# Performance work log

Hardware: AMD Instinct MI355X
Metric: run time of the kernel (lower is better)

The kernel has to match this reference:

```python
import jax, jax.numpy as jnp
import numpy as np

DIM = 192
HEADS = 6
WS = 8
SHIFT = 4
POS_DIM = 12  # (dim//4)//4
HIDDEN = 768
EPS = 1e-5


def _win_partition(x, ws):
    B, H, W, C = x.shape
    x = x.reshape(B, H // ws, ws, W // ws, ws, C)
    return x.transpose(0, 1, 3, 2, 4, 5).reshape(-1, ws, ws, C)


def _win_reverse(w, ws, H, W):
    B = w.shape[0] // ((H // ws) * (W // ws))
    x = w.reshape(B, H // ws, W // ws, ws, ws, -1)
    return x.transpose(0, 1, 3, 2, 4, 5).reshape(B, H, W, -1)


def _calc_mask(H, W, ws, shift):
    img = np.zeros((1, H, W, 1), np.float32)
    sl = (slice(0, -ws), slice(-ws, -shift), slice(-shift, None))
    cnt = 0
    for hs in sl:
        for wsl in sl:
            img[:, hs, wsl, :] = cnt
            cnt += 1
    mw = img.reshape(1, H // ws, ws, W // ws, ws, 1).transpose(0, 1, 3, 2, 4, 5).reshape(-1, ws * ws)
    am = mw[:, None, :] - mw[:, :, None]
    am = np.where(am != 0, -100.0, 0.0).astype(np.float32)
    return am  # [nW, N, N]


def _rel_index(ws):
    coords = np.stack(np.meshgrid(np.arange(ws), np.arange(ws), indexing='ij')).reshape(2, -1)
    rel = (coords[:, :, None] - coords[:, None, :]).transpose(1, 2, 0)
    rel[..., 0] += ws - 1
    rel[..., 1] += ws - 1
    rel[..., 0] *= 2 * ws - 1
    return rel.sum(-1)  # [N, N]


def _biases(ws):
    bh = np.arange(1 - ws, ws)
    bw = np.arange(1 - ws, ws)
    b = np.stack(np.meshgrid(bh, bw, indexing='ij')).reshape(2, -1).T
    return b.astype(np.float32)  # [(2ws-1)^2, 2]


def _ln(x, g, b):
    mu = jnp.mean(x, -1, keepdims=True)
    var = jnp.var(x, -1, keepdims=True)
    return (x - mu) / jnp.sqrt(var + EPS) * g + b


def setup_inputs() -> dict:
    key = jax.random.key(0)
    ks = jax.random.split(key, 20)
    B, L, C = 8, 128 * 128, DIM
    d = {
        'x': jax.random.normal(ks[0], (B, L, C), jnp.float32),
        'k_v': jnp.zeros((1,), jnp.float32),
        'H': 128, 'W': 128,
        'n1_g': jnp.ones((C,)), 'n1_b': jnp.zeros((C,)),
        'qkv_w': jax.random.normal(ks[1], (C, 3 * C)) * 0.02,
        'qkv_b': jnp.zeros((3 * C,)),
        'proj_w': jax.random.normal(ks[2], (C, C)) * 0.02,
        'proj_b': jnp.zeros((C,)),
        'pp_w': jax.random.normal(ks[3], (2, POS_DIM)) * 0.02,
        'pp_b': jnp.zeros((POS_DIM,)),
        'p1_g': jnp.ones((POS_DIM,)), 'p1_b': jnp.zeros((POS_DIM,)),
        'p1_w': jax.random.normal(ks[4], (POS_DIM, POS_DIM)) * 0.02,
        'p1_bias': jnp.zeros((POS_DIM,)),
        'p2_g': jnp.ones((POS_DIM,)), 'p2_b': jnp.zeros((POS_DIM,)),
        'p2_w': jax.random.normal(ks[5], (POS_DIM, POS_DIM)) * 0.02,
        'p2_bias': jnp.zeros((POS_DIM,)),
        'p3_g': jnp.ones((POS_DIM,)), 'p3_b': jnp.zeros((POS_DIM,)),
        'p3_w': jax.random.normal(ks[6], (POS_DIM, HEADS)) * 0.02,
        'p3_bias': jnp.zeros((HEADS,)),
        'n2_g': jnp.ones((C,)), 'n2_b': jnp.zeros((C,)),
        'fc1_w': jax.random.normal(ks[7], (C, HIDDEN)) * 0.02,
        'fc1_b': jnp.zeros((HIDDEN,)),
        'fc2_w': jax.random.normal(ks[8], (HIDDEN, C)) * 0.02,
        'fc2_b': jnp.zeros((C,)),
    }
    return d


def reference(x, k_v, H, W, n1_g, n1_b, qkv_w, qkv_b, proj_w, proj_b,
              pp_w, pp_b, p1_g, p1_b, p1_w, p1_bias, p2_g, p2_b, p2_w, p2_bias,
              p3_g, p3_b, p3_w, p3_bias, n2_g, n2_b, fc1_w, fc1_b, fc2_w, fc2_b):
    B, L, C = x.shape
    N = WS * WS
    hd = C // HEADS
    scale = hd ** (-0.5)

    rel_idx = jnp.asarray(_rel_index(WS).reshape(-1))            # [N*N]
    biases = jnp.asarray(_biases(WS))                            # [(2WS-1)^2, 2]
    mask = jnp.asarray(_calc_mask(H, W, WS, SHIFT))              # [nW, N, N]

    shortcut = x
    h = _ln(x, n1_g, n1_b).reshape(B, H, W, C)
    h = jnp.roll(h, (-SHIFT, -SHIFT), (1, 2))
    xw = _win_partition(h, WS).reshape(-1, N, C)                 # [B*nW, N, C]
    B_ = xw.shape[0]

    qkv = (xw @ qkv_w + qkv_b).reshape(B_, N, 3, HEADS, hd).transpose(2, 0, 3, 1, 4)
    q, k, v = qkv[0] * scale, qkv[1], qkv[2]                     # [B_, H, N, hd]
    attn = jnp.einsum('bhnd,bhmd->bhnm', q, k)

    # dynamic position bias MLP (residual=False path)
    pos = biases @ pp_w + pp_b
    pos = jax.nn.relu(_ln(pos, p1_g, p1_b)) @ p1_w + p1_bias
    pos = jax.nn.relu(_ln(pos, p2_g, p2_b)) @ p2_w + p2_bias
    pos = jax.nn.relu(_ln(pos, p3_g, p3_b)) @ p3_w + p3_bias     # [(2WS-1)^2, HEADS]
    rpb = pos[rel_idx].reshape(N, N, HEADS).transpose(2, 0, 1)   # [HEADS, N, N]
    attn = attn + rpb[None]

    nW = mask.shape[0]
    attn = attn.reshape(B_ // nW, nW, HEADS, N, N) + mask[None, :, None]
    attn = jax.nn.softmax(attn.reshape(-1, HEADS, N, N), axis=-1)

    out = jnp.einsum('bhnm,bhmd->bhnd', attn, v).transpose(0, 2, 1, 3).reshape(B_, N, C)
    out = out @ proj_w + proj_b

    out = _win_reverse(out.reshape(-1, WS, WS, C), WS, H, W)
    out = jnp.roll(out, (SHIFT, SHIFT), (1, 2)).reshape(B, L, C)

    y = shortcut + out
    m = _ln(y, n2_g, n2_b)
    m = jax.nn.gelu(m @ fc1_w + fc1_b, approximate=False) @ fc2_w + fc2_b
    return y + m
```

## Files before the change

kernel.cpp:

```cpp
#include <hip/hip_runtime.h>
#include <hip/hip_bf16.h>
#include <math.h>

using bf16 = __hip_bfloat16;

typedef __bf16 bf16x8 __attribute__((ext_vector_type(8)));
typedef float f32x4 __attribute__((ext_vector_type(4)));

__device__ __forceinline__ float bf2f(bf16 v) { return __bfloat162float(v); }
__device__ __forceinline__ bf16 f2bf(float v) { return __float2bfloat16(v); }
__device__ __forceinline__ float nz(float v) { return (v == v) ? v : 0.0f; }

__device__ __forceinline__ void gload_lds16(const void* g, void* l) {
    __builtin_amdgcn_global_load_lds(
        (const __attribute__((address_space(1))) unsigned int*)g,
        (__attribute__((address_space(3))) unsigned int*)l, 16, 0, 0);
}

__device__ __forceinline__ float fgelu(float v) {
    float z = v * (1.5957691f + 0.07135481f * v * v);
    return v / (1.0f + __expf(-z));
}

#define CDIM 192
#define NHEADS 6
#define ROWS 131072
#define HIDDEN 768

__global__ __launch_bounds__(256) void k_ln1_part(const float* __restrict__ x,
                                                  const float* __restrict__ g,
                                                  const float* __restrict__ bta,
                                                  bf16* __restrict__ xw) {
    int tid = threadIdx.x;
    int lane = tid & 63;
    int t = (blockIdx.x << 2) + (tid >> 6);
    int w = t >> 6, n = t & 63;
    int bb = w >> 8, wy = (w >> 4) & 15, wx = w & 15;
    int iy = n >> 3, ix = n & 7;
    int hs = (wy * 8 + iy + 4) & 127;
    int vs = (wx * 8 + ix + 4) & 127;
    const float* xr = x + ((size_t)bb * 16384 + (size_t)hs * 128 + vs) * CDIM;
    float v0 = nz(xr[lane]);
    float v1 = nz(xr[lane + 64]);
    float v2 = nz(xr[lane + 128]);
    float s = v0 + v1 + v2;
    float q = v0 * v0 + v1 * v1 + v2 * v2;
#pragma unroll
    for (int o = 32; o > 0; o >>= 1) { s += __shfl_xor(s, o); q += __shfl_xor(q, o); }
    float mean = s * (1.0f / 192.0f);
    float var = q * (1.0f / 192.0f) - mean * mean;
    float rs = rsqrtf(var + 1e-5f);
    bf16* orow = xw + (size_t)t * CDIM;
    orow[lane]       = f2bf((v0 - mean) * rs * g[lane]       + bta[lane]);
    orow[lane + 64]  = f2bf((v1 - mean) * rs * g[lane + 64]  + bta[lane + 64]);
    orow[lane + 128] = f2bf((v2 - mean) * rs * g[lane + 128] + bta[lane + 128]);
}

__global__ void k_transpose(const float* __restrict__ in, bf16* __restrict__ out, int K, int N) {
    int i = blockIdx.x * 256 + threadIdx.x;
    if (i < K * N) {
        int k = i / N, n = i - k * N;
        out[(size_t)n * K + k] = f2bf(in[i]);
    }
}

__global__ __launch_bounds__(256) void k_posmlp(
    const float* __restrict__ pp_w, const float* __restrict__ pp_b,
    const float* __restrict__ p1_g, const float* __restrict__ p1_b,
    const float* __restrict__ p1_w, const float* __restrict__ p1_bias,
    const float* __restrict__ p2_g, const float* __restrict__ p2_b,
    const float* __restrict__ p2_w, const float* __restrict__ p2_bias,
    const float* __restrict__ p3_g, const float* __restrict__ p3_b,
    const float* __restrict__ p3_w, const float* __restrict__ p3_bias,
    float* __restrict__ pos) {
    int i = threadIdx.x;
    if (i >= 225) return;
    float bh = (float)(i / 15 - 7), bw = (float)(i % 15 - 7);
    float v[12], u[12];
#pragma unroll
    for (int j = 0; j < 12; j++)
        v[j] = bh * pp_w[j] + bw * pp_w[12 + j] + pp_b[j];

    auto stage = [&](const float* gg, const float* bb2, const float* Wm, const float* bs, int OD) {
        float mean = 0.f;
        for (int j = 0; j < 12; j++) mean += v[j];
        mean *= (1.0f / 12.0f);
        float var = 0.f;
        for (int j = 0; j < 12; j++) { float d = v[j] - mean; var += d * d; }
        var *= (1.0f / 12.0f);
        float rs = rsqrtf(var + 1e-5f);
        for (int j = 0; j < 12; j++)
            u[j] = fmaxf((v[j] - mean) * rs * gg[j] + bb2[j], 0.0f);
        for (int o = 0; o < OD; o++) {
            float a = bs[o];
            for (int j = 0; j < 12; j++) a += u[j] * Wm[j * OD + o];
            v[o] = a;
        }
    };
    stage(p1_g, p1_b, p1_w, p1_bias, 12);
    stage(p2_g, p2_b, p2_w, p2_bias, 12);
    stage(p3_g, p3_b, p3_w, p3_bias, 6);
    for (int h = 0; h < 6; h++) pos[i * 6 + h] = v[h];
}

template <int EPI, typename OutT>
__global__ __launch_bounds__(256) void k_gemm(const bf16* __restrict__ A,
                                              const bf16* __restrict__ Bt,
                                              const float* __restrict__ bias,
                                              OutT* __restrict__ Cd,
                                              int M, int N, int K,
                                              const float* __restrict__ xres,
                                              const float* __restrict__ g2,
                                              const float* __restrict__ b2,
                                              float* __restrict__ yout,
                                              bf16* __restrict__ h2out) {
    constexpr int BM = 128, BN = 192, BK = 64;
    __shared__ __align__(16) unsigned short As[2][BM * BK];
    __shared__ __align__(16) unsigned short Bs[2][BN * BK];
    int tid = threadIdx.x;
    int wv = tid >> 6, lane = tid & 63;
    int lm = lane & 15, quad = lane >> 4;
    int sub = lane >> 3;
    int cb8 = (((lane & 7) ^ sub) << 3);
    int n0 = blockIdx.x * BN;
    int m0 = blockIdx.y * BM;

    const bf16* aSrc = A  + (size_t)(m0 + wv * 32 + sub) * K + cb8;
    const bf16* bSrc = Bt + (size_t)(n0 + wv * 48 + sub) * K + cb8;

    auto stage = [&](int buf, int k0) {
#pragma unroll
        for (int i = 0; i < 4; ++i)
            gload_lds16(aSrc + (size_t)(i * 8) * K + k0,
                        &As[buf][(wv * 32 + i * 8) * 64]);
#pragma unroll
        for (int i = 0; i < 6; ++i)
            gload_lds16(bSrc + (size_t)(i * 8) * K + k0,
                        &Bs[buf][(wv * 48 + i * 8) * 64]);
    };

    f32x4 acc[2][12] = {};

    auto compute = [&](int buf) {
#pragma unroll
        for (int ks = 0; ks < BK; ks += 32) {
            int xk = (ks + quad * 8) ^ ((lm & 7) << 3);
            bf16x8 af[2];
#pragma unroll
            for (int im = 0; im < 2; ++im)
                af[im] = *(const bf16x8*)&As[buf][(wv * 32 + im * 16 + lm) * 64 + xk];
#pragma unroll
            for (int in = 0; in < 12; ++in) {
                bf16x8 bq = *(const bf16x8*)&Bs[buf][(in * 16 + lm) * 64 + xk];
#pragma unroll
                for (int im = 0; im < 2; ++im)
                    acc[im][in] = __builtin_amdgcn_mfma_f32_16x16x32_bf16(
                        af[im], bq, acc[im][in], 0, 0, 0);
            }
        }
    };

    const int nt = K / BK;
    stage(0, 0);
    stage(1, BK);
    int cur = 0;
    for (int t = 0; t < nt; ++t) {
        if (t + 1 < nt)
            asm volatile("s_waitcnt vmcnt(10)" ::: "memory");
        else
            asm volatile("s_waitcnt vmcnt(0)" ::: "memory");
        __builtin_amdgcn_s_barrier();
        compute(cur);
        if (t + 2 < nt) {
            __builtin_amdgcn_s_barrier();
            stage(cur, (t + 2) * BK);
        }
        cur ^= 1;
    }

    if (EPI == 0) {
#pragma unroll
        for (int im = 0; im < 2; ++im) {
            int rbase = m0 + wv * 32 + im * 16 + quad * 4;
#pragma unroll
            for (int in = 0; in < 12; ++in) {
                int cg = n0 + in * 16 + lm;
                float bv = bias[cg];
#pragma unroll
                for (int r = 0; r < 4; ++r) {
                    float v = acc[im][in][r] + bv;
                    Cd[(size_t)(rbase + r) * N + cg] = (OutT)v;
                }
            }
        }
    } else {
#pragma unroll
        for (int im = 0; im < 2; ++im) {
            int rbase = m0 + wv * 32 + im * 16 + quad * 4;
#pragma unroll
            for (int r = 0; r < 4; ++r) {
                int grow = rbase + r;
                int w = grow >> 6, n = grow & 63;
                int bb = w >> 8, wy = (w >> 4) & 15, wx = w & 15;
                int iy = n >> 3, ix = n & 7;
                int hs = (wy * 8 + iy + 4) & 127;
                int vs = (wx * 8 + ix + 4) & 127;
                size_t xrow = ((size_t)bb * 16384 + (size_t)hs * 128 + vs) * 192;
                float vv[12];
                float s = 0.f, q = 0.f;
#pragma unroll
                for (int in = 0; in < 12; ++in) {
                    int col = in * 16 + lm;
                    float v = acc[im][in][r] + bias[col] + nz(xres[xrow + col]);
                    yout[xrow + col] = v;
                    vv[in] = v; s += v; q += v * v;
                }
#pragma unroll
                for (int o = 1; o < 16; o <<= 1) {
                    s += __shfl_xor(s, o); q += __shfl_xor(q, o);
                }
                float mean = s * (1.0f / 192.0f);
                float var = q * (1.0f / 192.0f) - mean * mean;
                float rsv = rsqrtf(var + 1e-5f);
#pragma unroll
                for (int in = 0; in < 12; ++in) {
                    int col = in * 16 + lm;
                    h2out[xrow + col] = f2bf((vv[in] - mean) * rsv * g2[col] + b2[col]);
                }
            }
        }
    }
}

__global__ __launch_bounds__(512) void k_mlp(const bf16* __restrict__ h2,
                                             const bf16* __restrict__ w1t,
                                             const float* __restrict__ b1,
                                             const bf16* __restrict__ w2t,
                                             const float* __restrict__ b2,
                                             float* __restrict__ y,
                                             int M) {
    __shared__ __align__(16) unsigned short Ah[3 * 128 * 64];
    __shared__ __align__(16) unsigned short Bb[2][192 * 64];
    __shared__ __align__(16) unsigned short Ps[3 * 128 * 64];
    __shared__ float b1s[HIDDEN];
    int tid = threadIdx.x;
    int wv = tid >> 6, lane = tid & 63;
    int lm = lane & 15, quad = lane >> 4;
    int sub = lane >> 3;
    int cb8 = (((lane & 7) ^ sub) << 3);
    int m0 = blockIdx.x * 128;

    for (int i = tid; i < HIDDEN; i += 512) b1s[i] = b1[i];

#pragma unroll
    for (int i = 0; i < 6; ++i) {
        int j = wv * 6 + i;
        int p = j >> 4, r0 = (j & 15) * 8;
        gload_lds16(h2 + (size_t)(m0 + r0 + sub) * 192 + p * 64 + cb8,
                    &Ah[p * 8192 + r0 * 64]);
    }

    auto stageChunk = [&](int c) {
        int kb = c / 6, ph = c % 6, slot = c & 1;
        if (ph < 3) {
            const bf16* s = w1t + (size_t)(kb * 192 + wv * 24 + sub) * 192 + ph * 64 + cb8;
#pragma unroll
            for (int i = 0; i < 3; ++i)
                gload_lds16(s + (size_t)(i * 8) * 192, &Bb[slot][(wv * 24 + i * 8) * 64]);
        } else {
            const bf16* s = w2t + (size_t)(wv * 24 + sub) * 768 + kb * 192 + (ph - 3) * 64 + cb8;
#pragma unroll
            for (int i = 0; i < 3; ++i)
                gload_lds16(s + (size_t)(i * 8) * 768, &Bb[slot][(wv * 24 + i * 8) * 64]);
        }
    };

    f32x4 a1[12];
    f32x4 a2[12] = {};

    auto docompute = [&](const unsigned short* Ap, int slot, f32x4 (&acc)[12]) {
#pragma unroll
        for (int ks = 0; ks < 64; ks += 32) {
            int xk = (ks + quad * 8) ^ ((lm & 7) << 3);
            bf16x8 af = *(const bf16x8*)&Ap[(wv * 16 + lm) * 64 + xk];
#pragma unroll
            for (int in = 0; in < 12; ++in) {
                bf16x8 bq = *(const bf16x8*)&Bb[slot][(in * 16 + lm) * 64 + xk];
                acc[in] = __builtin_amdgcn_mfma_f32_16x16x32_bf16(af, bq, acc[in], 0, 0, 0);
            }
        }
    };

    stageChunk(0);
    stageChunk(1);
    asm volatile("s_waitcnt lgkmcnt(0)" ::: "memory");

    for (int c = 0; c < 24; ++c) {
        if (c < 22)
            asm volatile("s_waitcnt vmcnt(3)" ::: "memory");
        else
            asm volatile("s_waitcnt vmcnt(0)" ::: "memory");
        __builtin_amdgcn_s_barrier();
        int kb = c / 6, ph = c % 6, slot = c & 1;
        if (ph == 0) {
#pragma unroll
            for (int in = 0; in < 12; ++in) a1[in] = (f32x4){0.f, 0.f, 0.f, 0.f};
        }
        if (ph < 3)
            docompute(&Ah[ph * 8192], slot, a1);
        else
            docompute(&Ps[(ph - 3) * 8192], slot, a2);
        __builtin_amdgcn_s_barrier();
        if (c + 2 < 24) stageChunk(c + 2);
        if (ph == 2) {
#pragma unroll
            for (int in = 0; in < 12; ++in) {
                int col = in * 16 + lm;
                float bv = b1s[kb * 192 + col];
                int plane = col >> 6, c6 = col & 63;
#pragma unroll
                for (int r = 0; r < 4; ++r) {
                    int rl = wv * 16 + quad * 4 + r;
                    float ge = fgelu(a1[in][r] + bv);
                    int sc = ((((c6 >> 3) ^ (rl & 7)) << 3) | (col & 7));
                    *(bf16*)&Ps[plane * 8192 + rl * 64 + sc] = f2bf(ge);
                }
            }
        }
    }

#pragma unroll
    for (int in = 0; in < 12; ++in) {
        int col = in * 16 + lm;
        float bv = b2[col];
#pragma unroll
        for (int r = 0; r < 4; ++r) {
            size_t o = (size_t)(m0 + wv * 16 + quad * 4 + r) * 192 + col;
            y[o] = a2[in][r] + bv + y[o];
        }
    }
}

__global__ __launch_bounds__(256) void k_attn(const bf16* __restrict__ qkv,
                                              const float* __restrict__ pos,
                                              bf16* __restrict__ outp) {
    __shared__ __align__(16) unsigned short Qs[64 * 40];
    __shared__ __align__(16) unsigned short Ks[64 * 40];
    __shared__ __align__(16) unsigned short Vt[32 * 72];
    __shared__ __align__(16) unsigned short Ps[64 * 72];
    int w = blockIdx.x, tid = threadIdx.x;
    int wv = tid >> 6, lane = tid & 63;
    int lm = lane & 15, quad = lane >> 4;
    int wy = (w >> 4) & 15, wx = w & 15;
    bool edge = (wy == 15) || (wx == 15);
    const float scale = 0.17677669529663687f;

    int srow = tid >> 2, scol = (tid & 3) << 3;
    const unsigned short* gq =
        (const unsigned short*)qkv + ((size_t)w * 64 + srow) * 576 + scol;

    int nbase = wv * 16 + quad * 4;

    for (int h = 0; h < 6; ++h) {
        uint4 uq = *(const uint4*)(gq + h * 32);
        uint4 uk = *(const uint4*)(gq + h * 32 + 192);
        uint4 uv = *(const uint4*)(gq + h * 32 + 384);
        *(uint4*)&Qs[srow * 40 + scol] = uq;
        *(uint4*)&Ks[srow * 40 + scol] = uk;
        const unsigned short* pv = (const unsigned short*)&uv;
#pragma unroll
        for (int j = 0; j < 8; j++) Vt[(scol + j) * 72 + srow] = pv[j];
        __syncthreads();

        f32x4 acc[4];
        bf16x8 af = *(const bf16x8*)&Qs[(wv * 16 + lm) * 40 + quad * 8];
#pragma unroll
        for (int ct = 0; ct < 4; ++ct) {
            bf16x8 bfk = *(const bf16x8*)&Ks[(ct * 16 + lm) * 40 + quad * 8];
            f32x4 z = {0.f, 0.f, 0.f, 0.f};
            acc[ct] = __builtin_amdgcn_mfma_f32_16x16x32_bf16(af, bfk, z, 0, 0, 0);
        }

        float sv[4][4];
#pragma unroll
        for (int ct = 0; ct < 4; ++ct) {
            int m = ct * 16 + lm;
            int iym = m >> 3, ixm = m & 7;
            int hm = wy * 8 + iym, wm = wx * 8 + ixm;
            int ridm = (hm < 120 ? 0 : (hm < 124 ? 1 : 2)) * 3 +
                       (wm < 120 ? 0 : (wm < 124 ? 1 : 2));
#pragma unroll
            for (int r = 0; r < 4; r++) {
                int n = nbase + r;
                int iyn = n >> 3, ixn = n & 7;
                float s = acc[ct][r] * scale +
                          pos[((iyn - iym + 7) * 15 + (ixn - ixm + 7)) * 6 + h];
                if (edge) {
                    int hn = wy * 8 + iyn, wn = wx * 8 + ixn;
                    int ridn = (hn < 120 ? 0 : (hn < 124 ? 1 : 2)) * 3 +
                               (wn < 120 ? 0 : (wn < 124 ? 1 : 2));
                    if (ridn != ridm) s -= 100.0f;
                }
                sv[ct][r] = s;
            }
        }

#pragma unroll
        for (int r = 0; r < 4; r++) {
            float mx = fmaxf(fmaxf(sv[0][r], sv[1][r]), fmaxf(sv[2][r], sv[3][r]));
#pragma unroll
            for (int o = 1; o < 16; o <<= 1) mx = fmaxf(mx, __shfl_xor(mx, o));
            float e0 = expf(sv[0][r] - mx), e1 = expf(sv[1][r] - mx);
            float e2 = expf(sv[2][r] - mx), e3 = expf(sv[3][r] - mx);
            float sum = e0 + e1 + e2 + e3;
#pragma unroll
            for (int o = 1; o < 16; o <<= 1) sum += __shfl_xor(sum, o);
            float inv = 1.0f / sum;
            int n = nbase + r;
            *(bf16*)&Ps[n * 72 + lm]      = f2bf(e0 * inv);
            *(bf16*)&Ps[n * 72 + 16 + lm] = f2bf(e1 * inv);
            *(bf16*)&Ps[n * 72 + 32 + lm] = f2bf(e2 * inv);
            *(bf16*)&Ps[n * 72 + 48 + lm] = f2bf(e3 * inv);
        }
        __syncthreads();

        f32x4 o0 = {0.f, 0.f, 0.f, 0.f}, o1 = {0.f, 0.f, 0.f, 0.f};
#pragma unroll
        for (int kc = 0; kc < 2; kc++) {
            bf16x8 pa = *(const bf16x8*)&Ps[(wv * 16 + lm) * 72 + kc * 32 + quad * 8];
            bf16x8 vb0 = *(const bf16x8*)&Vt[lm * 72 + kc * 32 + quad * 8];
            bf16x8 vb1 = *(const bf16x8*)&Vt[(16 + lm) * 72 + kc * 32 + quad * 8];
            o0 = __builtin_amdgcn_mfma_f32_16x16x32_bf16(pa, vb0, o0, 0, 0, 0);
            o1 = __builtin_amdgcn_mfma_f32_16x16x32_bf16(pa, vb1, o1, 0, 0, 0);
        }
#pragma unroll
        for (int r = 0; r < 4; r++) {
            int n = nbase + r;
            size_t base = ((size_t)w * 64 + n) * 192 + h * 32;
            outp[base + lm]      = f2bf(o0[r]);
            outp[base + 16 + lm] = f2bf(o1[r]);
        }
        __syncthreads();
    }
}

extern "C" void kernel_launch(void* const* d_in, const int* in_sizes, int n_in,
                              void* d_out, int out_size, void* d_ws, size_t ws_size,
                              hipStream_t stream) {
    (void)in_sizes; (void)n_in; (void)out_size;
    const float* x      = (const float*)d_in[0];
    const float* n1_g   = (const float*)d_in[4];
    const float* n1_b   = (const float*)d_in[5];
    const float* qkv_w  = (const float*)d_in[6];
    const float* qkv_b  = (const float*)d_in[7];
    const float* proj_w = (const float*)d_in[8];
    const float* proj_b = (const float*)d_in[9];
    const float* pp_w   = (const float*)d_in[10];
    const float* pp_b   = (const float*)d_in[11];
    const float* p1_g   = (const float*)d_in[12];
    const float* p1_b   = (const float*)d_in[13];
    const float* p1_w   = (const float*)d_in[14];
    const float* p1_bias= (const float*)d_in[15];
    const float* p2_g   = (const float*)d_in[16];
    const float* p2_b   = (const float*)d_in[17];
    const float* p2_w   = (const float*)d_in[18];
    const float* p2_bias= (const float*)d_in[19];
    const float* p3_g   = (const float*)d_in[20];
    const float* p3_b   = (const float*)d_in[21];
    const float* p3_w   = (const float*)d_in[22];
    const float* p3_bias= (const float*)d_in[23];
    const float* n2_g   = (const float*)d_in[24];
    const float* n2_b   = (const float*)d_in[25];
    const float* fc1_w  = (const float*)d_in[26];
    const float* fc1_b  = (const float*)d_in[27];
    const float* fc2_w  = (const float*)d_in[28];
    const float* fc2_b  = (const float*)d_in[29];

    char* ws = (char*)d_ws;
    size_t off = 0;
    auto alloc = [&](size_t bytes) -> char* {
        char* p = ws + off;
        off += (bytes + 255) & ~(size_t)255;
        return p;
    };
    bf16* qkvwT  = (bf16*)alloc((size_t)CDIM * 576 * 2);
    bf16* projwT = (bf16*)alloc((size_t)CDIM * CDIM * 2);
    bf16* fc1wT  = (bf16*)alloc((size_t)CDIM * HIDDEN * 2);
    bf16* fc2wT  = (bf16*)alloc((size_t)HIDDEN * CDIM * 2);
    float* pos   = (float*)alloc(225 * 6 * 4);

    const size_t flatNeed = (size_t)ROWS * CDIM * 2
                          + (size_t)ROWS * HIDDEN * 2
                          + (size_t)ROWS * CDIM * 2
                          + (1u << 20);
    const bool flat = (ws_size > off) && ((ws_size - off) >= flatNeed);
    const int NCH = flat ? 1 : 8;
    const int NIMG = flat ? 8 : 1;
    const size_t R = (size_t)16384 * NIMG;

    bf16 *xw_b, *qkv_buf, *attn_b, *h2_b;
    if (flat) {
        bf16* region0 = (bf16*)alloc((size_t)ROWS * CDIM * 2);
        bf16* region1 = (bf16*)alloc((size_t)ROWS * HIDDEN * 2);
        h2_b = (bf16*)alloc((size_t)ROWS * CDIM * 2);
        xw_b = attn_b = region0;
        qkv_buf = region1;
    } else {
        xw_b     = (bf16*)alloc(R * CDIM * 2);
        qkv_buf  = (bf16*)alloc(R * 576 * 2);
        attn_b   = (bf16*)alloc(R * CDIM * 2);
        h2_b     = (bf16*)alloc(R * CDIM * 2);
    }
    float* yout = (float*)d_out;

    k_transpose<<<(CDIM * 576 + 255) / 256, 256, 0, stream>>>(qkv_w, qkvwT, CDIM, 576);
    k_transpose<<<(CDIM * CDIM + 255) / 256, 256, 0, stream>>>(proj_w, projwT, CDIM, CDIM);
    k_transpose<<<(CDIM * HIDDEN + 255) / 256, 256, 0, stream>>>(fc1_w, fc1wT, CDIM, HIDDEN);
    k_transpose<<<(HIDDEN * CDIM + 255) / 256, 256, 0, stream>>>(fc2_w, fc2wT, HIDDEN, CDIM);
    k_posmlp<<<1, 256, 0, stream>>>(pp_w, pp_b, p1_g, p1_b, p1_w, p1_bias,
                                    p2_g, p2_b, p2_w, p2_bias,
                                    p3_g, p3_b, p3_w, p3_bias, pos);

    for (int c = 0; c < NCH; ++c) {
        const float* x_c = x + (size_t)c * 16384 * CDIM;
        float* y_c = yout + (size_t)c * 16384 * CDIM;

        k_ln1_part<<<(int)(R / 4), 256, 0, stream>>>(x_c, n1_g, n1_b, xw_b);

        k_gemm<0, bf16><<<dim3(576 / 192, (int)(R / 128)), 256, 0, stream>>>(
            xw_b, qkvwT, qkv_b, qkv_buf, (int)R, 576, CDIM,
            nullptr, nullptr, nullptr, nullptr, nullptr);

        k_attn<<<(int)(R / 64), 256, 0, stream>>>(qkv_buf, pos, attn_b);

        k_gemm<3, bf16><<<dim3(1, (int)(R / 128)), 256, 0, stream>>>(
            attn_b, projwT, proj_b, (bf16*)nullptr, (int)R, CDIM, CDIM,
            x_c, n2_g, n2_b, y_c, h2_b);

        k_mlp<<<(int)(R / 128), 512, 0, stream>>>(
            h2_b, fc1wT, fc1_b, fc2wT, fc2_b, y_c, (int)R);
    }
}
```

Before: 646.2 us.

## Shrink MLP block to 64 rows and keep A operand in registers

The fused MLP kernel now uses 256 threads handling 64 rows instead of 512 threads handling 128 rows. Each wave loads its LayerNorm-output A fragments straight into registers, removing the A tile from LDS. Each thread stages twice as many weight chunks, and the vmcnt wait is adjusted to match. This cuts LDS use and may allow higher occupancy, but each weight chunk is now reused by half as many rows, doubling weight traffic per row. GELU also replaces a divide with a hardware reciprocal.

```diff
diff --git a/kernel.cpp b/kernel.cpp
--- a/kernel.cpp
+++ b/kernel.cpp
@@ -19,7 +19,7 @@
 
 __device__ __forceinline__ float fgelu(float v) {
     float z = v * (1.5957691f + 0.07135481f * v * v);
-    return v / (1.0f + __expf(-z));
+    return v * __builtin_amdgcn_rcpf(1.0f + __expf(-z));
 }
 
 #define CDIM 192
@@ -232,64 +232,48 @@
     }
 }
 
-__global__ __launch_bounds__(512) void k_mlp(const bf16* __restrict__ h2,
+__global__ __launch_bounds__(256) void k_mlp(const bf16* __restrict__ h2,
                                              const bf16* __restrict__ w1t,
                                              const float* __restrict__ b1,
                                              const bf16* __restrict__ w2t,
                                              const float* __restrict__ b2,
                                              float* __restrict__ y,
                                              int M) {
-    __shared__ __align__(16) unsigned short Ah[3 * 128 * 64];
     __shared__ __align__(16) unsigned short Bb[2][192 * 64];
-    __shared__ __align__(16) unsigned short Ps[3 * 128 * 64];
+    __shared__ __align__(16) unsigned short Ps[3 * 64 * 64];
     __shared__ float b1s[HIDDEN];
     int tid = threadIdx.x;
     int wv = tid >> 6, lane = tid & 63;
     int lm = lane & 15, quad = lane >> 4;
     int sub = lane >> 3;
     int cb8 = (((lane & 7) ^ sub) << 3);
-    int m0 = blockIdx.x * 128;
-
-    for (int i = tid; i < HIDDEN; i += 512) b1s[i] = b1[i];
-
-#pragma unroll
-    for (int i = 0; i < 6; ++i) {
-        int j = wv * 6 + i;
-        int p = j >> 4, r0 = (j & 15) * 8;
-        gload_lds16(h2 + (size_t)(m0 + r0 + sub) * 192 + p * 64 + cb8,
-                    &Ah[p * 8192 + r0 * 64]);
-    }
+    int m0 = blockIdx.x * 64;
+
+    for (int i = tid; i < HIDDEN; i += 256) b1s[i] = b1[i];
+
+    const bf16* arow = h2 + (size_t)(m0 + wv * 16 + lm) * 192 + quad * 8;
+    bf16x8 af[6];
+#pragma unroll
+    for (int kk = 0; kk < 6; ++kk)
+        af[kk] = *(const bf16x8*)(arow + kk * 32);
 
     auto stageChunk = [&](int c) {
         int kb = c / 6, ph = c % 6, slot = c & 1;
         if (ph < 3) {
-            const bf16* s = w1t + (size_t)(kb * 192 + wv * 24 + sub) * 192 + ph * 64 + cb8;
-#pragma unroll
-            for (int i = 0; i < 3; ++i)
-                gload_lds16(s + (size_t)(i * 8) * 192, &Bb[slot][(wv * 24 + i * 8) * 64]);
+            const bf16* s = w1t + (size_t)(kb * 192 + wv * 48 + sub) * 192 + ph * 64 + cb8;
+#pragma unroll
+            for (int i = 0; i < 6; ++i)
+                gload_lds16(s + (size_t)(i * 8) * 192, &Bb[slot][(wv * 48 + i * 8) * 64]);
         } else {
-            const bf16* s = w2t + (size_t)(wv * 24 + sub) * 768 + kb * 192 + (ph - 3) * 64 + cb8;
-#pragma unroll
-            for (int i = 0; i < 3; ++i)
-                gload_lds16(s + (size_t)(i * 8) * 768, &Bb[slot][(wv * 24 + i * 8) * 64]);
+            const bf16* s = w2t + (size_t)(wv * 48 + sub) * 768 + kb * 192 + (ph - 3) * 64 + cb8;
+#pragma unroll
+            for (int i = 0; i < 6; ++i)
+                gload_lds16(s + (size_t)(i * 8) * 768, &Bb[slot][(wv * 48 + i * 8) * 64]);
         }
     };
 
     f32x4 a1[12];
     f32x4 a2[12] = {};
-
-    auto docompute = [&](const unsigned short* Ap, int slot, f32x4 (&acc)[12]) {
-#pragma unroll
-        for (int ks = 0; ks < 64; ks += 32) {
-            int xk = (ks + quad * 8) ^ ((lm & 7) << 3);
-            bf16x8 af = *(const bf16x8*)&Ap[(wv * 16 + lm) * 64 + xk];
-#pragma unroll
-            for (int in = 0; in < 12; ++in) {
-                bf16x8 bq = *(const bf16x8*)&Bb[slot][(in * 16 + lm) * 64 + xk];
-                acc[in] = __builtin_amdgcn_mfma_f32_16x16x32_bf16(af, bq, acc[in], 0, 0, 0);
-            }
-        }
-    };
 
     stageChunk(0);
     stageChunk(1);
@@ -297,7 +281,7 @@
 
     for (int c = 0; c < 24; ++c) {
         if (c < 22)
-            asm volatile("s_waitcnt vmcnt(3)" ::: "memory");
+            asm volatile("s_waitcnt vmcnt(6)" ::: "memory");
         else
             asm volatile("s_waitcnt vmcnt(0)" ::: "memory");
         __builtin_amdgcn_s_barrier();
@@ -306,10 +290,30 @@
 #pragma unroll
             for (int in = 0; in < 12; ++in) a1[in] = (f32x4){0.f, 0.f, 0.f, 0.f};
         }
-        if (ph < 3)
-            docompute(&Ah[ph * 8192], slot, a1);
-        else
-            docompute(&Ps[(ph - 3) * 8192], slot, a2);
+        if (ph < 3) {
+#pragma unroll
+            for (int ks = 0; ks < 2; ++ks) {
+                int xk = (ks * 32 + quad * 8) ^ ((lm & 7) << 3);
+                bf16x8 a = af[ph * 2 + ks];
+#pragma unroll
+                for (int in = 0; in < 12; ++in) {
+                    bf16x8 bq = *(const bf16x8*)&Bb[slot][(in * 16 + lm) * 64 + xk];
+                    a1[in] = __builtin_amdgcn_mfma_f32_16x16x32_bf16(a, bq, a1[in], 0, 0, 0);
+                }
+            }
+        } else {
+            const unsigned short* Ap = &Ps[(ph - 3) * 4096];
+#pragma unroll
+            for (int ks = 0; ks < 2; ++ks) {
+                int xk = (ks * 32 + quad * 8) ^ ((lm & 7) << 3);
+                bf16x8 a = *(const bf16x8*)&Ap[(wv * 16 + lm) * 64 + xk];
+#pragma unroll
+                for (int in = 0; in < 12; ++in) {
+                    bf16x8 bq = *(const bf16x8*)&Bb[slot][(in * 16 + lm) * 64 + xk];
+                    a2[in] = __builtin_amdgcn_mfma_f32_16x16x32_bf16(a, bq, a2[in], 0, 0, 0);
+                }
+            }
+        }
         __builtin_amdgcn_s_barrier();
         if (c + 2 < 24) stageChunk(c + 2);
         if (ph == 2) {
@@ -323,7 +327,7 @@
                     int rl = wv * 16 + quad * 4 + r;
                     float ge = fgelu(a1[in][r] + bv);
                     int sc = ((((c6 >> 3) ^ (rl & 7)) << 3) | (col & 7));
-                    *(bf16*)&Ps[plane * 8192 + rl * 64 + sc] = f2bf(ge);
+                    *(bf16*)&Ps[plane * 4096 + rl * 64 + sc] = f2bf(ge);
                 }
             }
         }
@@ -537,7 +541,7 @@
             attn_b, projwT, proj_b, (bf16*)nullptr, (int)R, CDIM, CDIM,
             x_c, n2_g, n2_b, y_c, h2_b);
 
-        k_mlp<<<(int)(R / 128), 512, 0, stream>>>(
+        k_mlp<<<(int)(R / 64), 256, 0, stream>>>(
             h2_b, fc1wT, fc1_b, fc2wT, fc2_b, y_c, (int)R);
     }
 }
```

Result: slower. 1.255 ms (+94.2%).
